# Optimization experiments

Measured on AMD Instinct MI355X. Metric: run time of the kernel, lower is better.

## Reference

```python
import jax, jax.numpy as jnp
import numpy as np

N = 65536          # rays per batch
NC = 64            # coarse samples (config.num_samples_coarse)
NF = 128           # fine samples (config.num_samples_fine)
NEAR, FAR = 0.1, 1000.0


def setup_inputs() -> dict:
    key = jax.random.key(0)
    k = jax.random.split(key, 7)
    ray_origins = jax.random.normal(k[0], (N, 3), jnp.float32)
    ray_directions = jax.random.normal(k[1], (N, 3), jnp.float32)
    # stratified coarse t_vals == sample_points_along_rays(stratified=True)
    t = NEAR + (FAR - NEAR) * jnp.linspace(0.0, 1.0, NC, dtype=jnp.float32)
    t = jnp.broadcast_to(t, (N, NC))
    mids = 0.5 * (t[:, 1:] + t[:, :-1])
    upper = jnp.concatenate([mids, t[:, -1:]], axis=-1)
    lower = jnp.concatenate([t[:, :1], mids], axis=-1)
    t_rand = jax.random.uniform(k[2], (N, NC), jnp.float32)
    coarse_t_vals = lower + (upper - lower) * t_rand
    coarse_weights = jax.random.uniform(k[3], (N, NC), jnp.float32)
    u = jax.random.uniform(k[4], (N, NF), jnp.float32)
    colors = jax.random.uniform(k[5], (N, NC + NF, 3), jnp.float32)
    densities = jax.random.uniform(k[6], (N, NC + NF, 1), jnp.float32)
    return {"ray_origins": ray_origins, "ray_directions": ray_directions,
            "coarse_weights": coarse_weights, "coarse_t_vals": coarse_t_vals,
            "u": u, "colors": colors, "densities": densities}


def _hierarchical_sampling(ray_origins, ray_directions, coarse_weights, coarse_t_vals, u):
    # inverse-CDF importance resampling (GridNeRFRenderer.hierarchical_sampling)
    w = coarse_weights + 1e-5
    pdf = w / jnp.sum(w, axis=-1, keepdims=True)                 # [N, NC]
    cdf = jnp.cumsum(pdf, axis=-1)
    cdf = jnp.concatenate([jnp.zeros_like(cdf[..., :1]), cdf], axis=-1)  # [N, NC+1]
    # per-ray searchsorted (right)
    indices = jax.vmap(lambda c, uu: jnp.searchsorted(c, uu, side="right"))(cdf, u)  # [N, NF]
    nc = coarse_t_vals.shape[-1]
    below = jnp.clip(indices - 1, 0, nc - 1)
    above = jnp.clip(indices, 0, nc - 1)
    cdf_b = jnp.take_along_axis(cdf, below, axis=1)
    cdf_a = jnp.take_along_axis(cdf, above, axis=1)
    t_b = jnp.take_along_axis(coarse_t_vals, below, axis=1)
    t_a = jnp.take_along_axis(coarse_t_vals, above, axis=1)
    denom = cdf_a - cdf_b
    denom = jnp.where(denom < 1e-5, jnp.ones_like(denom), denom)
    tt = (u - cdf_b) / denom
    fine_t_vals = t_b + tt * (t_a - t_b)
    combined_t_vals = jnp.sort(jnp.concatenate([coarse_t_vals, fine_t_vals], axis=-1), axis=-1)  # [N, NC+NF]
    fine_points = ray_origins[:, None, :] + ray_directions[:, None, :] * combined_t_vals[..., None]
    return fine_points, combined_t_vals


def _volume_rendering(colors, densities, t_vals, ray_directions):
    dists = t_vals[..., 1:] - t_vals[..., :-1]
    dists = jnp.concatenate([dists, jnp.full_like(dists[..., :1], 1e10)], axis=-1)
    dists = dists * jnp.linalg.norm(ray_directions, axis=-1, keepdims=True)   # [N, S]
    alpha = 1.0 - jnp.exp(-densities[..., 0] * dists)                         # [N, S]
    # exclusive cumprod transmittance (== cumprod + roll + T[...,0]=1)
    trans = jnp.cumprod(1.0 - alpha + 1e-10, axis=-1)
    trans = jnp.concatenate([jnp.ones_like(trans[..., :1]), trans[..., :-1]], axis=-1)
    weights = alpha * trans
    rgb = jnp.sum(weights[..., None] * colors, axis=-2)   # [N, 3]
    depth = jnp.sum(weights * t_vals, axis=-1)            # [N]
    opacity = jnp.sum(weights, axis=-1)                   # [N]
    return rgb, depth, opacity, weights


def reference(ray_origins, ray_directions, coarse_weights, coarse_t_vals, u, colors, densities):
    fine_points, combined_t_vals = _hierarchical_sampling(
        ray_origins, ray_directions, coarse_weights, coarse_t_vals, u)
    rgb, depth, opacity, weights = _volume_rendering(
        colors, densities, combined_t_vals, ray_directions)
    return (rgb, depth, opacity, fine_points)
```

## Files before the change

kernel.cpp:

```cpp
#include <hip/hip_runtime.h>
#include <math.h>


#define NRAYS 65536
#define NCC   64
#define NFF   128
#define SS    192

__global__ __launch_bounds__(256)
void nerf_fused(const float* __restrict__ ro,  const float* __restrict__ rd,
                const float* __restrict__ cw,  const float* __restrict__ ct,
                const float* __restrict__ uu,  const float* __restrict__ col,
                const float* __restrict__ den, float* __restrict__ out)
{
    const int lane = threadIdx.x & 63;
    const int wv   = threadIdx.x >> 6;
    const int ray  = blockIdx.x * 4 + wv;

    __shared__ float s_cdf[4][66];
    __shared__ float s_vals[4][256];

    float wt = cw[(size_t)ray * NCC + lane] + 1e-5f;
    float tc = ct[(size_t)ray * NCC + lane];
    float x = wt;
    #pragma unroll
    for (int off = 1; off < 64; off <<= 1) {
        float y = __shfl_up(x, off);
        if (lane >= off) x += y;
    }
    float total = __shfl(x, 63);
    s_cdf[wv][lane + 1] = x / total;
    if (lane == 0) s_cdf[wv][0] = 0.0f;
    s_vals[wv][lane] = tc;
    s_vals[wv][192 + lane] = 1e30f;
    __syncthreads();

    const float* cdfp = s_cdf[wv];
    const float* tcp  = s_vals[wv];
    float2 u2 = *(const float2*)(uu + (size_t)ray * NFF + 2 * lane);
    float fr[2];
    #pragma unroll
    for (int q = 0; q < 2; ++q) {
        float u = q ? u2.y : u2.x;
        int pos = 0;
        #pragma unroll
        for (int st = 32; st >= 1; st >>= 1) {
            int np = pos + st;
            pos = (cdfp[np] <= u) ? np : pos;
        }
        int below = pos;
        int above = (pos + 1 < 63) ? (pos + 1) : 63;
        float cb = cdfp[below];
        float ca = cdfp[above];
        float tb = tcp[below];
        float ta = tcp[above];
        float dnm = ca - cb;
        dnm = (dnm < 1e-5f) ? 1.0f : dnm;
        float tt = (u - cb) / dnm;
        fr[q] = tb + tt * (ta - tb);
    }
    *(float2*)&s_vals[wv][NCC + 2 * lane] = make_float2(fr[0], fr[1]);
    __syncthreads();

    float4 vv4 = *(const float4*)&s_vals[wv][4 * lane];
    float v[4] = {vv4.x, vv4.y, vv4.z, vv4.w};
    #pragma unroll
    for (int k = 2; k <= 256; k <<= 1) {
        #pragma unroll
        for (int j = k >> 1; j >= 1; j >>= 1) {
            if (j >= 4) {
                const int m = j >> 2;
                bool lower = (lane & m) == 0;
                #pragma unroll
                for (int r = 0; r < 4; ++r) {
                    bool up = ((((lane << 2) | r) & k) == 0);
                    float p = __shfl_xor(v[r], m);
                    float mn = fminf(v[r], p), mx = fmaxf(v[r], p);
                    v[r] = (lower == up) ? mn : mx;
                }
            } else if (j == 2) {
                #pragma unroll
                for (int r = 0; r < 2; ++r) {
                    bool up = ((((lane << 2) | r) & k) == 0);
                    float a = v[r], b = v[r + 2];
                    v[r]     = up ? fminf(a, b) : fmaxf(a, b);
                    v[r + 2] = up ? fmaxf(a, b) : fminf(a, b);
                }
            } else {
                #pragma unroll
                for (int r = 0; r < 4; r += 2) {
                    bool up = ((((lane << 2) | r) & k) == 0);
                    float a = v[r], b = v[r + 1];
                    v[r]     = up ? fminf(a, b) : fmaxf(a, b);
                    v[r + 1] = up ? fmaxf(a, b) : fminf(a, b);
                }
            }
        }
    }

    float dx = rd[(size_t)ray * 3 + 0], dy = rd[(size_t)ray * 3 + 1], dz = rd[(size_t)ray * 3 + 2];
    float ox = ro[(size_t)ray * 3 + 0], oy = ro[(size_t)ray * 3 + 1], oz = ro[(size_t)ray * 3 + 2];
    float nrm = sqrtf(dx * dx + dy * dy + dz * dz);

    const bool active = lane < 48;
    float tnext = __shfl_down(v[0], 1);
    float dd[4];
    dd[0] = v[1] - v[0];
    dd[1] = v[2] - v[1];
    dd[2] = v[3] - v[2];
    dd[3] = (lane == 47) ? 1e10f : (tnext - v[3]);

    float4 dn4 = make_float4(0.f, 0.f, 0.f, 0.f);
    if (active) dn4 = *(const float4*)(den + (size_t)ray * SS + 4 * lane);
    float dnv[4] = {dn4.x, dn4.y, dn4.z, dn4.w};

    float aa[4], ff[4];
    #pragma unroll
    for (int r = 0; r < 4; ++r) {
        float al = active ? (1.0f - expf(-dnv[r] * (dd[r] * nrm))) : 0.0f;
        aa[r] = al;
        ff[r] = active ? (1.0f - al + 1e-10f) : 1.0f;
    }

    if (active) {
        float* fp = out + (size_t)5 * NRAYS + (size_t)ray * (SS * 3) + 12 * lane;
        float4 p0 = make_float4(ox + dx * v[0], oy + dy * v[0], oz + dz * v[0], ox + dx * v[1]);
        float4 p1 = make_float4(oy + dy * v[1], oz + dz * v[1], ox + dx * v[2], oy + dy * v[2]);
        float4 p2 = make_float4(oz + dz * v[2], ox + dx * v[3], oy + dy * v[3], oz + dz * v[3]);
        *(float4*)(fp + 0) = p0;
        *(float4*)(fp + 4) = p1;
        *(float4*)(fp + 8) = p2;
    }

    float pr1 = ff[0], pr2 = ff[0] * ff[1], pr3 = pr2 * ff[2];
    float lp = pr3 * ff[3];
    float sx = lp;
    #pragma unroll
    for (int off = 1; off < 64; off <<= 1) {
        float y = __shfl_up(sx, off);
        if (lane >= off) sx *= y;
    }
    float excl = __shfl_up(sx, 1);
    if (lane == 0) excl = 1.0f;
    float w0 = aa[0] * excl;
    float w1 = aa[1] * (excl * pr1);
    float w2 = aa[2] * (excl * pr2);
    float w3 = aa[3] * (excl * pr3);

    float4 c0 = make_float4(0.f,0.f,0.f,0.f), c1 = c0, c2 = c0;
    if (active) {
        const float* cp = col + (size_t)ray * (SS * 3) + 12 * lane;
        c0 = *(const float4*)(cp + 0);
        c1 = *(const float4*)(cp + 4);
        c2 = *(const float4*)(cp + 8);
    }
    float rr  = w0 * c0.x + w1 * c0.w + w2 * c1.z + w3 * c2.y;
    float gg  = w0 * c0.y + w1 * c1.x + w2 * c1.w + w3 * c2.z;
    float bb  = w0 * c0.z + w1 * c1.y + w2 * c2.x + w3 * c2.w;
    float dep = w0 * v[0] + w1 * v[1] + w2 * v[2] + w3 * v[3];
    float opa = w0 + w1 + w2 + w3;

    #pragma unroll
    for (int off = 32; off >= 1; off >>= 1) {
        rr  += __shfl_xor(rr,  off);
        gg  += __shfl_xor(gg,  off);
        bb  += __shfl_xor(bb,  off);
        dep += __shfl_xor(dep, off);
        opa += __shfl_xor(opa, off);
    }
    if (lane == 0) {
        out[(size_t)ray * 3 + 0] = rr;
        out[(size_t)ray * 3 + 1] = gg;
        out[(size_t)ray * 3 + 2] = bb;
        out[(size_t)3 * NRAYS + ray] = dep;
        out[(size_t)4 * NRAYS + ray] = opa;
    }
}

extern "C" void kernel_launch(void* const* d_in, const int* in_sizes, int n_in,
                              void* d_out, int out_size, void* d_ws, size_t ws_size,
                              hipStream_t stream) {
    const float* ro  = (const float*)d_in[0];
    const float* rd  = (const float*)d_in[1];
    const float* cw  = (const float*)d_in[2];
    const float* ct  = (const float*)d_in[3];
    const float* uu  = (const float*)d_in[4];
    const float* col = (const float*)d_in[5];
    const float* den = (const float*)d_in[6];
    float* out = (float*)d_out;
    (void)in_sizes; (void)n_in; (void)out_size; (void)d_ws; (void)ws_size;
    nerf_fused<<<NRAYS / 4, 256, 0, stream>>>(ro, rd, cw, ct, uu, col, den, out);
}
```

Baseline: 348.9 us.

## Replace 256-element bitonic sort with sorted-u search and merge-by-rank placement

Drops the full 256-wide bitonic sort of coarse plus fine t values. It sorts only the 128 u samples with a two-per-lane bitonic network, then scatters each fine sample and each coarse sample straight to its final slot, using rank from the CDF binary search and from a binary search over the sorted u. The CDF is made monotone with a prefix max so the ranks stay consistent. This cuts shuffle and compare work, but it relies on the fine t values being monotone in u, and it removes the __syncthreads between the shared-memory writes and the cross-lane reads, which risks a data race.

```diff
diff --git a/kernel.cpp b/kernel.cpp
--- a/kernel.cpp
+++ b/kernel.cpp
@@ -17,7 +17,9 @@
     const int wv   = threadIdx.x >> 6;
     const int ray  = blockIdx.x * 4 + wv;
 
-    __shared__ float s_cdf[4][66];
+    __shared__ float s_cdf[4][65];
+    __shared__ float s_ct [4][64];
+    __shared__ float s_su [4][128];
     __shared__ float s_vals[4][256];
 
     float wt = cw[(size_t)ray * NCC + lane] + 1e-5f;
@@ -29,74 +31,76 @@
         if (lane >= off) x += y;
     }
     float total = __shfl(x, 63);
-    s_cdf[wv][lane + 1] = x / total;
+    float cv = x / total;
+    #pragma unroll
+    for (int off = 1; off < 64; off <<= 1) {
+        float y = __shfl_up(cv, off);
+        if (lane >= off) cv = fmaxf(cv, y);
+    }
+    s_cdf[wv][lane + 1] = cv;
     if (lane == 0) s_cdf[wv][0] = 0.0f;
-    s_vals[wv][lane] = tc;
-    s_vals[wv][192 + lane] = 1e30f;
-    __syncthreads();
+    s_ct[wv][lane] = tc;
+
+    float2 u2 = *(const float2*)(uu + (size_t)ray * NFF + 2 * lane);
+    float v0 = u2.x, v1 = u2.y;
+    #pragma unroll
+    for (int k = 2; k <= 128; k <<= 1) {
+        #pragma unroll
+        for (int j = k >> 1; j >= 1; j >>= 1) {
+            bool up = (((lane << 1) & k) == 0);
+            if (j == 1) {
+                float a = v0, b = v1;
+                v0 = up ? fminf(a, b) : fmaxf(a, b);
+                v1 = up ? fmaxf(a, b) : fminf(a, b);
+            } else {
+                int m = j >> 1;
+                bool keepmin = (((lane & m) == 0) == up);
+                float p0 = __shfl_xor(v0, m);
+                float p1 = __shfl_xor(v1, m);
+                v0 = keepmin ? fminf(v0, p0) : fmaxf(v0, p0);
+                v1 = keepmin ? fminf(v1, p1) : fmaxf(v1, p1);
+            }
+        }
+    }
+    *(float2*)&s_su[wv][2 * lane] = make_float2(v0, v1);
 
     const float* cdfp = s_cdf[wv];
-    const float* tcp  = s_vals[wv];
-    float2 u2 = *(const float2*)(uu + (size_t)ray * NFF + 2 * lane);
-    float fr[2];
+    const float* ctp  = s_ct[wv];
+    float us[2] = {v0, v1};
     #pragma unroll
     for (int q = 0; q < 2; ++q) {
-        float u = q ? u2.y : u2.x;
+        float u = us[q];
         int pos = 0;
         #pragma unroll
         for (int st = 32; st >= 1; st >>= 1) {
             int np = pos + st;
             pos = (cdfp[np] <= u) ? np : pos;
         }
-        int below = pos;
         int above = (pos + 1 < 63) ? (pos + 1) : 63;
-        float cb = cdfp[below];
-        float ca = cdfp[above];
-        float tb = tcp[below];
-        float ta = tcp[above];
+        float cb = cdfp[pos], ca = cdfp[above];
+        float tb = ctp[pos],  ta = ctp[above];
         float dnm = ca - cb;
         dnm = (dnm < 1e-5f) ? 1.0f : dnm;
         float tt = (u - cb) / dnm;
-        fr[q] = tb + tt * (ta - tb);
+        float fval = tb + tt * (ta - tb);
+        int rank = 2 * lane + q + pos + 1;
+        s_vals[wv][rank] = fval;
     }
-    *(float2*)&s_vals[wv][NCC + 2 * lane] = make_float2(fr[0], fr[1]);
-    __syncthreads();
 
-    float4 vv4 = *(const float4*)&s_vals[wv][4 * lane];
-    float v[4] = {vv4.x, vv4.y, vv4.z, vv4.w};
+    const float* sup = s_su[wv];
+    float key = cdfp[lane];
+    int cnt = 0;
     #pragma unroll
-    for (int k = 2; k <= 256; k <<= 1) {
-        #pragma unroll
-        for (int j = k >> 1; j >= 1; j >>= 1) {
-            if (j >= 4) {
-                const int m = j >> 2;
-                bool lower = (lane & m) == 0;
-                #pragma unroll
-                for (int r = 0; r < 4; ++r) {
-                    bool up = ((((lane << 2) | r) & k) == 0);
-                    float p = __shfl_xor(v[r], m);
-                    float mn = fminf(v[r], p), mx = fmaxf(v[r], p);
-                    v[r] = (lower == up) ? mn : mx;
-                }
-            } else if (j == 2) {
-                #pragma unroll
-                for (int r = 0; r < 2; ++r) {
-                    bool up = ((((lane << 2) | r) & k) == 0);
-                    float a = v[r], b = v[r + 2];
-                    v[r]     = up ? fminf(a, b) : fmaxf(a, b);
-                    v[r + 2] = up ? fmaxf(a, b) : fminf(a, b);
-                }
-            } else {
-                #pragma unroll
-                for (int r = 0; r < 4; r += 2) {
-                    bool up = ((((lane << 2) | r) & k) == 0);
-                    float a = v[r], b = v[r + 1];
-                    v[r]     = up ? fminf(a, b) : fmaxf(a, b);
-                    v[r + 1] = up ? fmaxf(a, b) : fminf(a, b);
-                }
-            }
-        }
+    for (int st = 128; st >= 1; st >>= 1) {
+        int np = cnt + st;
+        bool ok = (np <= 128) && (sup[np - 1] < key);
+        cnt = ok ? np : cnt;
     }
+    s_vals[wv][lane + cnt] = tc;
+    s_vals[wv][192 + lane] = 0.0f;
+
+    float4 sv = *(const float4*)&s_vals[wv][4 * lane];
+    float v[4] = {sv.x, sv.y, sv.z, sv.w};
 
     float dx = rd[(size_t)ray * 3 + 0], dy = rd[(size_t)ray * 3 + 1], dz = rd[(size_t)ray * 3 + 2];
     float ox = ro[(size_t)ray * 3 + 0], oy = ro[(size_t)ray * 3 + 1], oz = ro[(size_t)ray * 3 + 2];
@@ -133,8 +137,7 @@
     }
 
     float pr1 = ff[0], pr2 = ff[0] * ff[1], pr3 = pr2 * ff[2];
-    float lp = pr3 * ff[3];
-    float sx = lp;
+    float sx = pr3 * ff[3];
     #pragma unroll
     for (int off = 1; off < 64; off <<= 1) {
         float y = __shfl_up(sx, off);
```

Result: no change. 344.9 us (-1.2%).
